# Optimization experiments

Hardware: AMD Instinct MI355X
Metric: run time of the kernel (lower is better)

Reference implementation:

```python
import jax, jax.numpy as jnp
import numpy as np

B, N, K = 2, 8192, 9
FEAT_C, COST_C, FLOW_C = 128, 64, 3
CH = [128, 128]          # PointConv output channels
MLP = [128, 64]          # pointwise Conv1d channels
WN = 16                  # WeightNet output width
HID = [8, 8]             # WeightNet hidden widths
SLOPE = 0.1              # leaky relu slope
EPS = 1e-5
CLAMP = (-200.0, 200.0)


def setup_inputs() -> dict:
    key = jax.random.key(0)
    ks = iter(jax.random.split(key, 64))
    def nrm(shape, s=0.02):
        return jax.random.normal(next(ks), shape, jnp.float32) * s
    inp = {}
    inp["xyz"] = jax.random.normal(next(ks), (B, N, 3), jnp.float32)
    inp["feats"] = jax.random.normal(next(ks), (B, FEAT_C, N), jnp.float32)
    inp["cost_volume"] = jax.random.normal(next(ks), (B, COST_C, N), jnp.float32)
    inp["flow"] = jax.random.normal(next(ks), (B, FLOW_C, N), jnp.float32)
    last = FEAT_C + COST_C + FLOW_C
    for i, co in enumerate(CH):
        cin = last + 3
        p = f"pc{i}_"
        inp[p + "w1"] = nrm((HID[0], 3)); inp[p + "b1"] = jnp.zeros((HID[0],), jnp.float32)
        inp[p + "w2"] = nrm((HID[1], HID[0])); inp[p + "b2"] = jnp.zeros((HID[1],), jnp.float32)
        inp[p + "w3"] = nrm((WN, HID[1])); inp[p + "b3"] = jnp.zeros((WN,), jnp.float32)
        inp[p + "linW"] = nrm((co, cin * WN)); inp[p + "linb"] = jnp.zeros((co,), jnp.float32)
        last = co
    for i, co in enumerate(MLP):
        inp[f"mlp{i}_W"] = nrm((co, last)); inp[f"mlp{i}_b"] = jnp.zeros((co,), jnp.float32)
        last = co
    inp["fc_W"] = nrm((3, last)); inp["fc_b"] = jnp.zeros((3,), jnp.float32)
    return inp


def _bn(x, axes):
    m = x.mean(axes, keepdims=True)
    v = x.var(axes, keepdims=True)
    return (x - m) / jnp.sqrt(v + EPS)


def _leaky(x):
    return jnp.where(x >= 0, x, SLOPE * x)


def _knn_idx(xyz, k):
    # xyz: [B,N,3] -> idx [B,N,K] of k nearest (incl. self)
    sq = jnp.sum(xyz * xyz, -1)                       # [B,N]
    d = sq[:, :, None] + sq[:, None, :] - 2.0 * jnp.einsum('bnc,bmc->bnm', xyz, xyz)
    return jax.lax.top_k(-d, k)[1]                    # [B,N,K]


def _gather(a, idx):
    # a: [B,N,C], idx: [B,N,K] -> [B,N,K,C]
    return jax.vmap(lambda x, i: x[i])(a, idx)


def _pointconv(xyz, points, idx, w1, b1, w2, b2, w3, b3, linW, linb):
    # xyz [B,N,3], points [B,C,N] -> [B,out,N]
    g_xyz = _gather(xyz, idx) - xyz[:, :, None, :]    # [B,N,K,3] relative coords
    g_pts = _gather(jnp.transpose(points, (0, 2, 1)), idx)  # [B,N,K,C]
    grouped = jnp.concatenate([g_pts, g_xyz], -1)     # [B,N,K,C+3]
    # WeightNet on relative coords: 3 -> 8 -> 8 -> 16 (bn+relu each)
    h = jax.nn.relu(_bn(g_xyz @ w1.T + b1, (0, 1, 2)))
    h = jax.nn.relu(_bn(h @ w2.T + b2, (0, 1, 2)))
    w = jax.nn.relu(_bn(h @ w3.T + b3, (0, 1, 2)))    # [B,N,K,WN]
    bsz, n = grouped.shape[0], grouped.shape[1]
    agg = jnp.einsum('bnkc,bnkw->bncw', grouped, w).reshape(bsz, n, -1)
    out = agg @ linW.T + linb                         # [B,N,out]
    out = _leaky(_bn(out, (0, 1)))
    return jnp.transpose(out, (0, 2, 1))              # [B,out,N]


def reference(xyz, feats, cost_volume, flow,
              pc0_w1, pc0_b1, pc0_w2, pc0_b2, pc0_w3, pc0_b3, pc0_linW, pc0_linb,
              pc1_w1, pc1_b1, pc1_w2, pc1_b2, pc1_w3, pc1_b3, pc1_linW, pc1_linb,
              mlp0_W, mlp0_b, mlp1_W, mlp1_b, fc_W, fc_b):
    idx = _knn_idx(xyz, K)
    x = jnp.concatenate([feats, cost_volume, flow], axis=1)  # [B, feat+cost+flow, N]
    x = _pointconv(xyz, x, idx, pc0_w1, pc0_b1, pc0_w2, pc0_b2, pc0_w3, pc0_b3, pc0_linW, pc0_linb)
    x = _pointconv(xyz, x, idx, pc1_w1, pc1_b1, pc1_w2, pc1_b2, pc1_w3, pc1_b3, pc1_linW, pc1_linb)
    x = _leaky(jnp.einsum('oc,bcn->bon', mlp0_W, x) + mlp0_b[None, :, None])
    x = _leaky(jnp.einsum('oc,bcn->bon', mlp1_W, x) + mlp1_b[None, :, None])
    fl = jnp.einsum('oc,bcn->bon', fc_W, x) + fc_b[None, :, None]
    return x, jnp.clip(fl, CLAMP[0], CLAMP[1])
```

## Files before the change

kernel.cpp:

```cpp
#include <hip/hip_runtime.h>

#define NBATCH 2
#define NPTS   8192
#define NPT    (NBATCH*NPTS)
#define KNN    9
#define SEG    32
#define SEGN   (NPTS/SEG)
#define SCAP   8
#define SSTR   9

typedef unsigned short u16;
typedef unsigned int   u32;
typedef short bf16x8 __attribute__((ext_vector_type(8)));
typedef float f32x4  __attribute__((ext_vector_type(4)));

__device__ __forceinline__ float wred(float v){
#pragma unroll
  for(int o=32;o>0;o>>=1) v += __shfl_down(v,o);
  return v;
}

__device__ __forceinline__ u16 f2b(float f){
  u32 u = __float_as_uint(f);
  return (u16)((u + 0x7fffu + ((u>>16)&1u)) >> 16);
}

__device__ __forceinline__ float bumpup(float x){
  u32 u = __float_as_uint(x);
  if(u == 0x80000000u) u = 1u;
  else if((int)u >= 0) u += 1u;
  else u -= 1u;
  return __uint_as_float(u);
}

__global__ __launch_bounds__(256) void k_build_xin(
    const float* __restrict__ feats, const float* __restrict__ cost,
    const float* __restrict__ flow, const float* __restrict__ xyz,
    float* __restrict__ xin, float4* __restrict__ xs)
{
  __shared__ float buf[196][67];
  int t = threadIdx.x;
  int pt0 = blockIdx.x*64;
  int b = pt0 >> 13, n0 = pt0 & (NPTS-1);
  int lane = t & 63, grp = t >> 6;
  const float* f  = feats + (size_t)b*128*NPTS + n0 + lane;
  const float* cv = cost  + (size_t)b*64 *NPTS + n0 + lane;
  const float* fl = flow  + (size_t)b*3  *NPTS + n0 + lane;
  for(int c=grp; c<128; c+=4) buf[c][lane]      = f[(size_t)c*NPTS];
  for(int c=grp; c<64;  c+=4) buf[128+c][lane]  = cv[(size_t)c*NPTS];
  if(grp<3) buf[192+grp][lane] = fl[(size_t)grp*NPTS];
  else      buf[195][lane] = 0.f;
  if(t < 64){
    int pt = pt0 + t;
    const float* p = xyz + (size_t)b*NPTS*3 + 3*(pt & (NPTS-1));
    float x=p[0], y=p[1], z=p[2];
    float s = __fadd_rn(__fadd_rn(__fmul_rn(x,x),__fmul_rn(y,y)),__fmul_rn(z,z));
    xs[pt] = make_float4(x,y,z,s);
  }
  __syncthreads();
  for(int e=t; e<64*49; e+=256){
    int p = e/49, q = e-p*49;
    float4 v = make_float4(buf[4*q][p], buf[4*q+1][p], buf[4*q+2][p], buf[4*q+3][p]);
    *(float4*)(xin + (size_t)(pt0+p)*196 + 4*q) = v;
  }
}

__global__ __launch_bounds__(256) void k_thr(
    const float4* __restrict__ xs, float* __restrict__ thr)
{
  __shared__ float md[4][64][9];
  int t = threadIdx.x, lane = t & 63, wave = t >> 6;
  int qb = blockIdx.x;
  int b = qb >> 7;
  int n = (qb & 127)*64 + lane;
  const float4* xb4 = xs + (size_t)b*NPTS;
  float4 q = xb4[n];
  float qx=q.x, qy=q.y, qz=q.z, qs=q.w;
  float bd[KNN];
#pragma unroll
  for(int i=0;i<KNN;i++) bd[i]=__builtin_inff();
  for(int i=0;i<128;i++){
    int m = (wave*128 + i)*16;
    float4 c = xb4[m];
    float dot = fmaf(c.z,qz, fmaf(c.y,qy, __fmul_rn(c.x,qx)));
    float d = __fsub_rn(__fadd_rn(qs,c.w), __fmul_rn(2.0f,dot));
    if(d < bd[KNN-1]){
      bd[KNN-1]=d;
#pragma unroll
      for(int r=KNN-2;r>=0;r--){
        if(bd[r+1] < bd[r]){ float td=bd[r]; bd[r]=bd[r+1]; bd[r+1]=td; }
      }
    }
  }
#pragma unroll
  for(int i=0;i<KNN;i++) md[wave][lane][i]=bd[i];
  __syncthreads();
  if(t < 64){
    float b2[KNN];
#pragma unroll
    for(int i=0;i<KNN;i++) b2[i]=__builtin_inff();
    for(int w=0;w<4;w++){
#pragma unroll
      for(int i=0;i<KNN;i++){
        float d = md[w][t][i];
        if(d < b2[KNN-1]){
          b2[KNN-1]=d;
#pragma unroll
          for(int r=KNN-2;r>=0;r--){
            if(b2[r+1] < b2[r]){ float td=b2[r]; b2[r]=b2[r+1]; b2[r+1]=td; }
          }
        }
      }
    }
    thr[(b<<13) + (qb & 127)*64 + t] = b2[KNN-1];
  }
}

__global__ __launch_bounds__(256) void k_knn_part(
    const float4* __restrict__ xs, const float* __restrict__ thr,
    int* __restrict__ pi)
{
  __shared__ int sqi[256*SSTR];
  int t = threadIdx.x;
  int seg = blockIdx.x & (SEG-1);
  int qc  = blockIdx.x >> 5;
  int b = qc >> 5;
  int n = (qc & 31)*256 + t;
  int pt = (b<<13) + n;
  const float4* xb4 = xs + (size_t)b*NPTS;
  float4 q = xb4[n];
  float qx=q.x, qy=q.y, qz=q.z, qs=q.w;
  float init = bumpup(thr[pt]);
  float bd[KNN]; int bi[KNN];
#pragma unroll
  for(int i=0;i<KNN;i++){ bd[i]=init; bi[i]=0x7fffffff; }
  float cut = init;
  int cnt = 0;
  int* msi = sqi + t*SSTR;
  auto flush = [&](){
    for(int i=0;i<cnt;i++){
      int id = msi[i];
      float4 c = xb4[id];
      float dot = fmaf(c.z,qz, fmaf(c.y,qy, __fmul_rn(c.x,qx)));
      float d = __fsub_rn(__fadd_rn(qs,c.w), __fmul_rn(2.0f,dot));
      if(d < bd[KNN-1]){
        bd[KNN-1]=d; bi[KNN-1]=id;
#pragma unroll
        for(int r=KNN-2;r>=0;r--){
          if(bd[r+1] < bd[r]){
            float td=bd[r]; bd[r]=bd[r+1]; bd[r+1]=td;
            int ti=bi[r]; bi[r]=bi[r+1]; bi[r+1]=ti;
          }
        }
      }
    }
    cnt = 0;
    cut = bd[KNN-1];
  };
  const int m0 = seg*SEGN;
  for(int j0=0; j0<SEGN; j0+=8){
    float dv[8];
#pragma unroll
    for(int u=0;u<8;u++){
      float4 c = xb4[m0+j0+u];
      float dot = fmaf(c.z,qz, fmaf(c.y,qy, __fmul_rn(c.x,qx)));
      dv[u] = __fsub_rn(__fadd_rn(qs,c.w), __fmul_rn(2.0f,dot));
    }
#pragma unroll
    for(int u=0;u<8;u++){
      if(dv[u] < cut){
        msi[cnt] = m0+j0+u; cnt++;
        if(cnt==SCAP) flush();
      }
    }
  }
  flush();
  size_t base = ((size_t)pt*SEG + seg)*KNN;
#pragma unroll
  for(int i=0;i<KNN;i++) pi[base+i]=bi[i];
}

__global__ __launch_bounds__(256) void k_knn_merge(
    const float4* __restrict__ xs, const int* __restrict__ pi,
    int* __restrict__ idxo, float* __restrict__ gpart)
{
  __shared__ float red[4][9];
  int t = threadIdx.x;
  int pt = blockIdx.x*256 + t;
  int b = pt >> 13;
  const float4* xb4 = xs + (size_t)b*NPTS;
  float4 q = xb4[pt & (NPTS-1)];
  float qx=q.x, qy=q.y, qz=q.z, qs=q.w;
  const int4* ip = (const int4*)(pi + (size_t)pt*SEG*KNN);
  float bd[KNN]; int bi[KNN];
#pragma unroll
  for(int i=0;i<KNN;i++){ bd[i]=__builtin_inff(); bi[i]=0x7fffffff; }
  for(int v=0; v<SEG*KNN/4; v++){
    int4 iv = ip[v];
    int ii[4] = {iv.x,iv.y,iv.z,iv.w};
#pragma unroll
    for(int u=0;u<4;u++){
      int id = ii[u];
      if(id != 0x7fffffff){
        float4 c = xb4[id];
        float dot = fmaf(c.z,qz, fmaf(c.y,qy, __fmul_rn(c.x,qx)));
        float d = __fsub_rn(__fadd_rn(qs,c.w), __fmul_rn(2.0f,dot));
        if(d < bd[KNN-1]){
          bd[KNN-1]=d; bi[KNN-1]=id;
#pragma unroll
          for(int i=KNN-2;i>=0;i--){
            if(bd[i+1] < bd[i]){
              float td=bd[i]; bd[i]=bd[i+1]; bd[i+1]=td;
              int ti=bi[i]; bi[i]=bi[i+1]; bi[i+1]=ti;
            }
          }
        }
      }
    }
  }
#pragma unroll
  for(int r=0;r<KNN;r++) idxo[pt*KNN + r] = bi[r];
  float mom[9];
#pragma unroll
  for(int i=0;i<9;i++) mom[i]=0.f;
#pragma unroll
  for(int r=0;r<KNN;r++){
    int m = bi[r];
    float4 c = xb4[m];
    float gx=c.x-qx, gy=c.y-qy, gz=c.z-qz;
    mom[0]+=gx; mom[1]+=gy; mom[2]+=gz;
    mom[3]=fmaf(gx,gx,mom[3]); mom[4]=fmaf(gy,gy,mom[4]); mom[5]=fmaf(gz,gz,mom[5]);
    mom[6]=fmaf(gx,gy,mom[6]); mom[7]=fmaf(gx,gz,mom[7]); mom[8]=fmaf(gy,gz,mom[8]);
  }
  int wave = t>>6, lane = t&63;
#pragma unroll
  for(int i=0;i<9;i++){
    float s = wred(mom[i]);
    if(lane==0) red[wave][i]=s;
  }
  __syncthreads();
  if(t<9)
    gpart[blockIdx.x*9 + t] = red[0][t]+red[1][t]+red[2][t]+red[3][t];
}

__global__ __launch_bounds__(256) void k_wn23a2(
    const float* __restrict__ xyz, const int* __restrict__ idx,
    const float* __restrict__ gpart, float cnt,
    const float* __restrict__ W1a, const float* __restrict__ B1a,
    const float* __restrict__ W2a, const float* __restrict__ B2a,
    const float* __restrict__ W1b, const float* __restrict__ B1b,
    const float* __restrict__ W2b, const float* __restrict__ B2b,
    float* __restrict__ houta, float* __restrict__ houtb,
    float* __restrict__ parta, float* __restrict__ partb)
{
  __shared__ float mom[9];
  __shared__ float stl[2][16];
  __shared__ float red[4][2][8];
  int t = threadIdx.x;
  if(t<9){
    float s=0.f;
    for(int r=0;r<64;r++) s += gpart[r*9+t];
    mom[t]=s;
  }
  __syncthreads();
  if(t<16){
    int L = t>>3, j = t&7;
    const float* W1 = L? W1b : W1a;
    const float* B1 = L? B1b : B1a;
    float inv = 1.0f/cnt;
    float w0=W1[3*j], w1=W1[3*j+1], w2=W1[3*j+2], bb=B1[j];
    float Eg0=mom[0]*inv, Eg1=mom[1]*inv, Eg2=mom[2]*inv;
    float Mxx=mom[3]*inv, Myy=mom[4]*inv, Mzz=mom[5]*inv;
    float Mxy=mom[6]*inv, Mxz=mom[7]*inv, Myz=mom[8]*inv;
    float mu_lin = w0*Eg0 + w1*Eg1 + w2*Eg2;
    float mean = mu_lin + bb;
    float e2 = w0*w0*Mxx + w1*w1*Myy + w2*w2*Mzz
             + 2.f*(w0*w1*Mxy + w0*w2*Mxz + w1*w2*Myz)
             + 2.f*bb*mu_lin + bb*bb;
    float var = e2 - mean*mean;
    stl[L][j] = mean;
    stl[L][8+j] = 1.0f/sqrtf(var + 1e-5f);
  }
  __syncthreads();
  int e = blockIdx.x*256 + t;
  int pt = e/KNN;
  int b = pt>>13, n = pt & (NPTS-1);
  int m = idx[e];
  const float* xb = xyz + (size_t)b*NPTS*3;
  float gx = xb[3*m]-xb[3*n], gy = xb[3*m+1]-xb[3*n+1], gz = xb[3*m+2]-xb[3*n+2];
  int wave = t>>6, lane = t&63;
#pragma unroll
  for(int L=0; L<2; L++){
    const float* W1 = L? W1b : W1a;
    const float* B1 = L? B1b : B1a;
    const float* W2 = L? W2b : W2a;
    const float* B2 = L? B2b : B2a;
    float* hout = L? houtb : houta;
    float* part = L? partb : parta;
    float x[8];
#pragma unroll
    for(int j=0;j<8;j++){
      float d = fmaf(gz, W1[3*j+2], fmaf(gy, W1[3*j+1], gx*W1[3*j]));
      float v = d + B1[j];
      v = (v - stl[L][j])*stl[L][8+j];
      x[j] = v>0.f? v : 0.f;
    }
    float v[8];
#pragma unroll
    for(int j=0;j<8;j++){
      float d = 0.f;
#pragma unroll
      for(int i=0;i<8;i++) d = fmaf(x[i], W2[j*8+i], d);
      v[j] = d + B2[j];
      hout[(size_t)e*8 + j] = v[j];
    }
#pragma unroll
    for(int j=0;j<8;j++){
      float s = wred(v[j]);
      float q = wred(v[j]*v[j]);
      if(lane==0){ red[wave][0][j]=s; red[wave][1][j]=q; }
    }
    __syncthreads();
    if(t < 16){
      int isq = t>>3, c = t&7;
      part[blockIdx.x*16 + t] =
        red[0][isq][c]+red[1][isq][c]+red[2][isq][c]+red[3][isq][c];
    }
    __syncthreads();
  }
}

__global__ __launch_bounds__(256) void k_wn23_2(
    const float* __restrict__ hina, const float* __restrict__ pina,
    const float* __restrict__ hinb, const float* __restrict__ pinb,
    int nb, float cnt,
    const float* __restrict__ Wa, const float* __restrict__ Ba,
    const float* __restrict__ Wb, const float* __restrict__ Bb,
    float* __restrict__ houta, float* __restrict__ houtb,
    float* __restrict__ parta, float* __restrict__ partb)
{
  __shared__ float sa[256], qa[256];
  __shared__ float stl[16];
  __shared__ float red[4][2][16];
  int t = threadIdx.x;
  int e = blockIdx.x*256 + t;
  int wave = t>>6, lane = t&63;
#pragma unroll
  for(int L=0; L<2; L++){
    const float* hin = L? hinb : hina;
    const float* pin = L? pinb : pina;
    const float* W   = L? Wb : Wa;
    const float* Bv  = L? Bb : Ba;
    float* hout = L? houtb : houta;
    float* part = L? partb : parta;
    {
      int c = t % 8;
      int r0 = t / 8;
      float s=0.f, q=0.f;
      for(int r=r0; r<nb; r+=32){
        s += pin[r*16 + c];
        q += pin[r*16 + 8 + c];
      }
      sa[t]=s; qa[t]=q;
      __syncthreads();
      if(t < 8){
        for(int g=1; g<32; g++){ s += sa[t+g*8]; q += qa[t+g*8]; }
        float mean = s/cnt;
        float var  = q/cnt - mean*mean;
        stl[t]   = mean;
        stl[8+t] = 1.0f/sqrtf(var + 1e-5f);
      }
      __syncthreads();
    }
    float x[8];
#pragma unroll
    for(int i=0;i<8;i++){
      float v = (hin[(size_t)e*8 + i] - stl[i])*stl[8+i];
      x[i] = v>0.f? v : 0.f;
    }
    float v[16];
#pragma unroll
    for(int j=0;j<16;j++){
      float d = 0.f;
#pragma unroll
      for(int i=0;i<8;i++) d = fmaf(x[i], W[j*8+i], d);
      v[j] = d + Bv[j];
      hout[(size_t)e*16 + j] = v[j];
    }
#pragma unroll
    for(int j=0;j<16;j++){
      float s = wred(v[j]);
      float q = wred(v[j]*v[j]);
      if(lane==0){ red[wave][0][j]=s; red[wave][1][j]=q; }
    }
    __syncthreads();
    if(t < 32){
      int isq = t>>4, c = t&15;
      part[blockIdx.x*32 + t] =
        red[0][isq][c]+red[1][isq][c]+red[2][isq][c]+red[3][isq][c];
    }
    __syncthreads();
  }
}

__global__ __launch_bounds__(256) void k_fin2(
    const float* __restrict__ pa, const float* __restrict__ pb,
    float* __restrict__ sta, float* __restrict__ stb, int nb, float cnt)
{
  __shared__ float sa[256], qa[256];
  int t = threadIdx.x;
  const int C = 16;
#pragma unroll
  for(int L=0; L<2; L++){
    const float* partial = L? pb : pa;
    float* st = L? stb : sta;
    int c = t % C;
    int r0 = t / C;
    int stride = 256 / C;
    float s=0.f, q=0.f;
    for(int r=r0; r<nb; r+=stride){
      s += partial[r*2*C + c];
      q += partial[r*2*C + C + c];
    }
    sa[t]=s; qa[t]=q;
    __syncthreads();
    if(t < C){
      for(int g=1; g<stride; g++){ s += sa[t+g*C]; q += qa[t+g*C]; }
      float mean = s/cnt;
      float var  = q/cnt - mean*mean;
      st[t]   = mean;
      st[C+t] = 1.0f/sqrtf(var + 1e-5f);
    }
    __syncthreads();
  }
}

__global__ __launch_bounds__(256) void k_fin(
    const float* __restrict__ partial, float* __restrict__ st,
    int C, int nb, float cnt)
{
  __shared__ float sa[256], qa[256];
  int t = threadIdx.x;
  int c = t % C;
  int r0 = t / C;
  int stride = 256 / C;
  float s=0.f, q=0.f;
  for(int r=r0; r<nb; r+=stride){
    s += partial[r*2*C + c];
    q += partial[r*2*C + C + c];
  }
  sa[t]=s; qa[t]=q;
  __syncthreads();
  if(t < C){
    for(int g=1; g<stride; g++){ s += sa[t+g*C]; q += qa[t+g*C]; }
    float mean = s/cnt;
    float var  = q/cnt - mean*mean;
    st[t]   = mean;
    st[C+t] = 1.0f/sqrtf(var + 1e-5f);
  }
}

__global__ __launch_bounds__(256) void k_prepW2(
    const float* __restrict__ W0, u16* __restrict__ Wh0,
    const float* __restrict__ W1, u16* __restrict__ Wh1)
{
  int e = blockIdx.x*256 + threadIdx.x;
  const int N0 = 128*3200;
  if(e < N0){
    int o = e / 3200, k = e - o*3200;
    float w = (k < 3168) ? W0[o*3168 + k] : 0.f;
    Wh0[e] = f2b(w);
  } else {
    int e1 = e - N0;
    if(e1 >= 128*2112) return;
    int o = e1 / 2112, k = e1 - o*2112;
    float w = (k < 2096) ? W1[o*2096 + k] : 0.f;
    Wh1[e1] = f2b(w);
  }
}

template<int CIN, int XSTRIDE, int KP, bool BN>
__global__ __launch_bounds__(256) void k_buildA(
    const float* __restrict__ xin, const float* __restrict__ xyz,
    const int* __restrict__ idx, const float* __restrict__ wpre,
    const float* __restrict__ st3, const float* __restrict__ bnst,
    u16* __restrict__ Abuf, int c0)
{
  constexpr int P = 16;
  constexpr int CPTS = CIN-3;
  constexpr int CPAD = KP/16;
  __shared__ float wm[P][KNN][16];
  __shared__ float gxs[P][KNN][3];
  __shared__ int   si[P][KNN];
  __shared__ float sm3[16], sr3[16];
  int t = threadIdx.x;
  int pt0 = c0 + blockIdx.x*P;
  int b = pt0 >> 13;
  const float* xb = xyz + (size_t)b*NPTS*3;
  if(t<16){ sm3[t]=st3[t]; sr3[t]=st3[16+t]; }
  for(int e=t; e<P*KNN; e+=256){
    int p = e/KNN, k = e - p*KNN;
    int n = (pt0+p)&(NPTS-1);
    int m = idx[(pt0+p)*KNN+k];
    si[p][k]=m;
    gxs[p][k][0]=xb[3*m]  -xb[3*n];
    gxs[p][k][1]=xb[3*m+1]-xb[3*n+1];
    gxs[p][k][2]=xb[3*m+2]-xb[3*n+2];
  }
  __syncthreads();
  for(int e=t; e<P*KNN*16; e+=256){
    int p = e/(KNN*16); int r = e - p*(KNN*16); int k = r>>4, wn = r&15;
    float v = (wpre[((size_t)(pt0+p)*KNN + k)*16 + wn] - sm3[wn]) * sr3[wn];
    wm[p][k][wn] = v>0.f? v:0.f;
  }
  __syncthreads();
  for(int it=t; it<P*CPAD; it+=256){
    int p = it/CPAD, c = it - p*CPAD;
    u32 u[8];
    if(c < CIN){
      float g[KNN];
      if(c < CPTS){
#pragma unroll
        for(int k=0;k<KNN;k++)
          g[k] = xin[(size_t)((b<<13) + si[p][k])*XSTRIDE + c];
        if(BN){
          float sm = bnst[c], sr = bnst[128+c];
#pragma unroll
          for(int k=0;k<KNN;k++){
            float v = (g[k]-sm)*sr;
            g[k] = v>=0.f? v : 0.1f*v;
          }
        }
      } else {
        int cc = c - CPTS;
#pragma unroll
        for(int k=0;k<KNN;k++) g[k] = gxs[p][k][cc];
      }
      float a[16];
#pragma unroll
      for(int wn=0; wn<16; wn++){
        float s = 0.f;
#pragma unroll
        for(int k=0;k<KNN;k++) s = fmaf(g[k], wm[p][k][wn], s);
        a[wn] = s;
      }
#pragma unroll
      for(int j=0;j<8;j++)
        u[j] = (u32)f2b(a[2*j]) | ((u32)f2b(a[2*j+1])<<16);
    } else {
#pragma unroll
      for(int j=0;j<8;j++) u[j]=0;
    }
    u32* dst = (u32*)(Abuf + ((size_t)(blockIdx.x*P + p)*KP + c*16));
    *(uint4*)dst       = make_uint4(u[0],u[1],u[2],u[3]);
    *((uint4*)dst + 1) = make_uint4(u[4],u[5],u[6],u[7]);
  }
}

__device__ __forceinline__ void gload16(const void* g, void* l){
  __builtin_amdgcn_global_load_lds(
      (const __attribute__((address_space(1))) u32*)g,
      (__attribute__((address_space(3))) u32*)l, 16, 0, 0);
}

template<int KP>
__global__ __launch_bounds__(512) void k_gemm(
    const u16* __restrict__ Wh, const u16* __restrict__ A,
    const float* __restrict__ linb, float* __restrict__ outp,
    float* __restrict__ partial, int ptBase)
{
  __shared__ __attribute__((aligned(16))) u16 lds[24576];
  constexpr int NT = KP/64;
  int t = threadIdx.x, wave = t>>6, lane = t&63;
  int p0 = blockIdx.x*64;
  const u16* Ab = A + (size_t)p0*KP;

  auto stage = [&](const u16* __restrict__ g, int k0, int ldsByteOff, int rows){
    int nr = (rows*128) >> 13;
    for(int r=0;r<nr;r++){
      int y  = (r*8 + wave) << 10;
      int yl = y + lane*16;
      int row = yl >> 7;
      int s = (yl >> 4) & 7;
      int c = s ^ (row & 7);
      const u16* src = g + (size_t)row*KP + k0 + c*8;
      gload16(src, (char*)lds + ldsByteOff + y);
    }
  };

  stage(Wh, 0, 0,     128);
  stage(Ab, 0, 32768, 64);

  f32x4 acc[4];
#pragma unroll
  for(int j=0;j<4;j++) acc[j]=(f32x4)(0.f);

  for(int kt=0; kt<NT; kt++){
    int cur = kt & 1;
    __syncthreads();
    if(kt+1 < NT){
      int nxt = cur^1;
      stage(Wh, (kt+1)*64, nxt*16384,         128);
      stage(Ab, (kt+1)*64, 32768 + nxt*8192,  64);
    }
    const u16* Lw = lds + cur*8192;
    const u16* La = lds + 16384 + cur*4096;
#pragma unroll
    for(int kf=0; kf<2; kf++){
      int cb = kf*4 + (lane>>4);
      bf16x8 af[4];
#pragma unroll
      for(int nf=0; nf<4; nf++){
        int p = nf*16 + (lane&15);
        af[nf] = *(const bf16x8*)(La + p*64 + ((cb ^ (p&7))<<3));
      }
      int row = wave*16 + (lane&15);
      bf16x8 wh = *(const bf16x8*)(Lw + row*64 + ((cb ^ (row&7))<<3));
#pragma unroll
      for(int nf=0; nf<4; nf++)
        acc[nf] = __builtin_amdgcn_mfma_f32_16x16x32_bf16(wh, af[nf], acc[nf], 0,0,0);
    }
  }

  int gb = (ptBase>>6) + blockIdx.x;
  int q = lane>>4, lc = lane&15;
  int obase = wave*16 + q*4;
#pragma unroll
  for(int r=0;r<4;r++){
    int o = obase + r;
    float bo = linb[o];
    float sv = 0.f, qv = 0.f;
#pragma unroll
    for(int nf=0; nf<4; nf++){
      float x = acc[nf][r] + bo;
      outp[(size_t)(ptBase + p0 + nf*16 + lc)*128 + o] = x;
      sv += x; qv = fmaf(x,x,qv);
    }
#pragma unroll
    for(int off=8; off>0; off>>=1){
      sv += __shfl_down(sv,off);
      qv += __shfl_down(qv,off);
    }
    if(lc==0){
      partial[gb*256 + o]       = sv;
      partial[gb*256 + 128 + o] = qv;
    }
  }
}

__global__ __launch_bounds__(512) void k_mlp(
    const float* __restrict__ outp1, const float* __restrict__ sto,
    const float* __restrict__ W0, const float* __restrict__ B0,
    const float* __restrict__ W1, const float* __restrict__ B1,
    const float* __restrict__ Wf, const float* __restrict__ Bf,
    float* __restrict__ dout)
{
  __shared__ float w0l[128*129];
  __shared__ float w1l[128*65];
  __shared__ float xt [128*65];
  __shared__ float m1l[64*65];
  int t = threadIdx.x;
  int pt0 = blockIdx.x*64;
  int b = pt0 >> 13, n0 = pt0 & (NPTS-1);
  for(int e=t; e<128*128; e+=512){ int o=e>>7, j=e&127; w0l[j*129+o] = W0[e]; }
  for(int e=t; e<64*128;  e+=512){ int o=e>>7, j=e&127; w1l[j*65+o]  = W1[e]; }
  for(int e=t; e<64*128;  e+=512){
    int p=e>>7, j=e&127;
    float v = outp1[(size_t)(pt0+p)*128 + j];
    v = (v - sto[j])*sto[128+j];
    xt[j*65+p] = v>=0.f? v : 0.1f*v;
  }
  __syncthreads();
  int p = t&63, wv = t>>6;
  float acc[16];
#pragma unroll
  for(int i=0;i<16;i++) acc[i]=0.f;
  for(int j=0;j<128;j++){
    float xv = xt[j*65+p];
#pragma unroll
    for(int i=0;i<16;i++)
      acc[i] = fmaf(w0l[j*129 + wv*16 + i], xv, acc[i]);
  }
  __syncthreads();
#pragma unroll
  for(int i=0;i<16;i++){
    int o = wv*16+i;
    float v = acc[i] + B0[o];
    v = v>=0.f? v : 0.1f*v;
    xt[o*65 + p] = v;
  }
  __syncthreads();
  float a2[8];
#pragma unroll
  for(int i=0;i<8;i++) a2[i]=0.f;
  for(int j=0;j<128;j++){
    float xv = xt[j*65+p];
#pragma unroll
    for(int i=0;i<8;i++)
      a2[i] = fmaf(w1l[j*65 + wv*8 + i], xv, a2[i]);
  }
#pragma unroll
  for(int i=0;i<8;i++){
    int o = wv*8+i;
    float v = a2[i] + B1[o];
    v = v>=0.f? v : 0.1f*v;
    dout[(size_t)(b*64+o)*NPTS + n0 + p] = v;
    m1l[o*65+p] = v;
  }
  __syncthreads();
  if(t < 192){
    int o = t/64, pp = t%64;
    float a = Bf[o];
    for(int j=0;j<64;j++) a = fmaf(Wf[o*64+j], m1l[j*65+pp], a);
    a = fminf(fmaxf(a, -200.f), 200.f);
    dout[(size_t)NBATCH*64*NPTS + (size_t)(b*3+o)*NPTS + n0 + pp] = a;
  }
}

extern "C" void kernel_launch(void* const* d_in, const int* in_sizes, int n_in,
                              void* d_out, int out_size, void* d_ws, size_t ws_size,
                              hipStream_t stream)
{
  (void)in_sizes; (void)n_in; (void)out_size;
  const float* xyz   = (const float*)d_in[0];
  const float* feats = (const float*)d_in[1];
  const float* cost  = (const float*)d_in[2];
  const float* flow  = (const float*)d_in[3];
  const float* pw1[2]  = {(const float*)d_in[4],  (const float*)d_in[12]};
  const float* pb1[2]  = {(const float*)d_in[5],  (const float*)d_in[13]};
  const float* pw2[2]  = {(const float*)d_in[6],  (const float*)d_in[14]};
  const float* pb2[2]  = {(const float*)d_in[7],  (const float*)d_in[15]};
  const float* pw3[2]  = {(const float*)d_in[8],  (const float*)d_in[16]};
  const float* pb3[2]  = {(const float*)d_in[9],  (const float*)d_in[17]};
  const float* plW[2]  = {(const float*)d_in[10], (const float*)d_in[18]};
  const float* plb[2]  = {(const float*)d_in[11], (const float*)d_in[19]};
  const float* m0W = (const float*)d_in[20];
  const float* m0b = (const float*)d_in[21];
  const float* m1W = (const float*)d_in[22];
  const float* m1b = (const float*)d_in[23];
  const float* fcW = (const float*)d_in[24];
  const float* fcb = (const float*)d_in[25];
  float* out = (float*)d_out;

  const int KP0 = 3200;
  const int KP1 = 2112;

  float* ws = (float*)d_ws;
  size_t o = 0;
  float* xin0 = ws + o; o += (size_t)NPT*196;
  int*   idx  = (int*)(ws + o); o += (size_t)NPT*KNN + 3;
  o &= ~(size_t)3;
  float4* xs  = (float4*)(ws + o); o += (size_t)NPT*4;
  float* thr  = ws + o; o += (size_t)NPT;
  int*   pi   = (int*)(ws + o); o += (size_t)NPT*SEG*KNN;
  float* h2a  = ws + o; o += (size_t)NPT*KNN*8;
  float* h2b  = ws + o; o += (size_t)NPT*KNN*8;
  float* wpre0 = ws + o; o += (size_t)NPT*KNN*16;
  float* wpre1 = ws + o; o += (size_t)NPT*KNN*16;
  float* gpart = ws + o; o += 64*9 + 7;
  float* part2a = ws + o; o += 576*16;
  float* part2b = ws + o; o += 576*16;
  float* part3a = ws + o; o += 576*32;
  float* part3b = ws + o; o += 576*32;
  float* parto = ws + o; o += 65536;
  float* st3a = ws + o; o += 32;
  float* st3b = ws + o; o += 32;
  float* sto0 = ws + o; o += 256;
  float* sto1 = ws + o; o += 256;
  float* outp0 = ws + o; o += (size_t)NPT*128;
  float* outp1 = ws + o; o += (size_t)NPT*128;
  u16* Wh0 = (u16*)(ws + o); o += (size_t)128*KP0/2;
  u16* Wh1 = (u16*)(ws + o); o += (size_t)128*KP1/2;
  u16* Abuf = (u16*)(ws + o);
  size_t used_bytes = o*4;
  size_t avail = ws_size > used_bytes ? ws_size - used_bytes : 0;
  int npc = NPT;
  while(npc > 1024 && (size_t)npc*KP0*2 > avail) npc >>= 1;

  k_build_xin<<<NPT/64, 256, 0, stream>>>(feats, cost, flow, xyz, xin0, xs);
  k_thr<<<256, 256, 0, stream>>>(xs, thr);
  k_knn_part<<<64*SEG, 256, 0, stream>>>(xs, thr, pi);
  k_knn_merge<<<NPT/256, 256, 0, stream>>>(xs, pi, idx, gpart);

  k_prepW2<<<(128*(KP0+KP1)+255)/256, 256, 0, stream>>>(plW[0], Wh0, plW[1], Wh1);

  const float cnt1 = (float)(NPT*KNN);
  const float cnto = (float)NPT;

  k_wn23a2<<<576,256,0,stream>>>(xyz, idx, gpart, cnt1,
                                 pw1[0], pb1[0], pw2[0], pb2[0],
                                 pw1[1], pb1[1], pw2[1], pb2[1],
                                 h2a, h2b, part2a, part2b);
  k_wn23_2<<<576,256,0,stream>>>(h2a, part2a, h2b, part2b, 576, cnt1,
                                 pw3[0], pb3[0], pw3[1], pb3[1],
                                 wpre0, wpre1, part3a, part3b);
  k_fin2<<<1,256,0,stream>>>(part3a, part3b, st3a, st3b, 576, cnt1);

  for(int c0 = 0; c0 < NPT; c0 += npc){
    k_buildA<198,196,KP0,false><<<npc/16,256,0,stream>>>(xin0, xyz, idx, wpre0, st3a, sto0, Abuf, c0);
    k_gemm<KP0><<<npc/64,512,0,stream>>>(Wh0, Abuf, plb[0], outp0, parto, c0);
  }
  k_fin<<<1,256,0,stream>>>(parto, sto0, 128, NPT/64, cnto);

  for(int c0 = 0; c0 < NPT; c0 += npc){
    k_buildA<131,128,KP1,true><<<npc/16,256,0,stream>>>(outp0, xyz, idx, wpre1, st3b, sto0, Abuf, c0);
    k_gemm<KP1><<<npc/64,512,0,stream>>>(Wh1, Abuf, plb[1], outp1, parto, c0);
  }
  k_fin<<<1,256,0,stream>>>(parto, sto1, 128, NPT/64, cnto);

  k_mlp<<<NPT/64,512,0,stream>>>(outp1, sto1, m0W,m0b, m1W,m1b, fcW,fcb, out);
}
```

Measured before the change: 580.1 us.

## Restructure KNN stages: finer threshold split, fewer segments, cache candidate distances

The threshold kernel now gives each query 16 threads instead of 4, so it launches more blocks and fills the GPU better. The partial KNN pass drops from 32 to 16 segments and keeps candidate distances in shared memory, so flushes no longer reload coordinates or recompute distances. It also writes partial distances along with indices, which lets the merge kernel skip its own gathers and distance math. In exchange there is an extra distance buffer in global memory, more shared memory per block, and each segment scans longer.

```diff
diff --git a/kernel.cpp b/kernel.cpp
--- a/kernel.cpp
+++ b/kernel.cpp
@@ -4,10 +4,9 @@
 #define NPTS   8192
 #define NPT    (NBATCH*NPTS)
 #define KNN    9
-#define SEG    32
+#define SEG    16
 #define SEGN   (NPTS/SEG)
-#define SCAP   8
-#define SSTR   9
+#define SSTR   20
 
 typedef unsigned short u16;
 typedef unsigned int   u32;
@@ -68,19 +67,20 @@
 __global__ __launch_bounds__(256) void k_thr(
     const float4* __restrict__ xs, float* __restrict__ thr)
 {
-  __shared__ float md[4][64][9];
-  int t = threadIdx.x, lane = t & 63, wave = t >> 6;
+  __shared__ float md[16][16][9];
+  int t = threadIdx.x;
+  int q = t & 15, chunk = t >> 4;
   int qb = blockIdx.x;
-  int b = qb >> 7;
-  int n = (qb & 127)*64 + lane;
+  int b = qb >> 9;
+  int n = (qb & 511)*16 + q;
   const float4* xb4 = xs + (size_t)b*NPTS;
-  float4 q = xb4[n];
-  float qx=q.x, qy=q.y, qz=q.z, qs=q.w;
+  float4 Q = xb4[n];
+  float qx=Q.x, qy=Q.y, qz=Q.z, qs=Q.w;
   float bd[KNN];
 #pragma unroll
   for(int i=0;i<KNN;i++) bd[i]=__builtin_inff();
-  for(int i=0;i<128;i++){
-    int m = (wave*128 + i)*16;
+  for(int i=0;i<32;i++){
+    int m = (chunk*32 + i)*16;
     float4 c = xb4[m];
     float dot = fmaf(c.z,qz, fmaf(c.y,qy, __fmul_rn(c.x,qx)));
     float d = __fsub_rn(__fadd_rn(qs,c.w), __fmul_rn(2.0f,dot));
@@ -93,16 +93,16 @@
     }
   }
 #pragma unroll
-  for(int i=0;i<KNN;i++) md[wave][lane][i]=bd[i];
-  __syncthreads();
-  if(t < 64){
+  for(int i=0;i<KNN;i++) md[q][chunk][i]=bd[i];
+  __syncthreads();
+  if(t < 16){
     float b2[KNN];
 #pragma unroll
     for(int i=0;i<KNN;i++) b2[i]=__builtin_inff();
-    for(int w=0;w<4;w++){
+    for(int w=0;w<16;w++){
 #pragma unroll
       for(int i=0;i<KNN;i++){
-        float d = md[w][t][i];
+        float d = md[t][w][i];
         if(d < b2[KNN-1]){
           b2[KNN-1]=d;
 #pragma unroll
@@ -112,18 +112,19 @@
         }
       }
     }
-    thr[(b<<13) + (qb & 127)*64 + t] = b2[KNN-1];
+    thr[(b<<13) + (qb & 511)*16 + t] = b2[KNN-1];
   }
 }
 
 __global__ __launch_bounds__(256) void k_knn_part(
     const float4* __restrict__ xs, const float* __restrict__ thr,
-    int* __restrict__ pi)
-{
-  __shared__ int sqi[256*SSTR];
+    float* __restrict__ pd, int* __restrict__ pi)
+{
+  __shared__ float sdq[256*SSTR];
+  __shared__ int   sqi[256*SSTR];
   int t = threadIdx.x;
   int seg = blockIdx.x & (SEG-1);
-  int qc  = blockIdx.x >> 5;
+  int qc  = blockIdx.x >> 4;
   int b = qc >> 5;
   int n = (qc & 31)*256 + t;
   int pt = (b<<13) + n;
@@ -136,13 +137,11 @@
   for(int i=0;i<KNN;i++){ bd[i]=init; bi[i]=0x7fffffff; }
   float cut = init;
   int cnt = 0;
-  int* msi = sqi + t*SSTR;
+  float* msd = sdq + t*SSTR;
+  int*   msi = sqi + t*SSTR;
   auto flush = [&](){
     for(int i=0;i<cnt;i++){
-      int id = msi[i];
-      float4 c = xb4[id];
-      float dot = fmaf(c.z,qz, fmaf(c.y,qy, __fmul_rn(c.x,qx)));
-      float d = __fsub_rn(__fadd_rn(qs,c.w), __fmul_rn(2.0f,dot));
+      float d = msd[i]; int id = msi[i];
       if(d < bd[KNN-1]){
         bd[KNN-1]=d; bi[KNN-1]=id;
 #pragma unroll
@@ -159,6 +158,7 @@
   };
   const int m0 = seg*SEGN;
   for(int j0=0; j0<SEGN; j0+=8){
+    if(cnt > SSTR-8) flush();
     float dv[8];
 #pragma unroll
     for(int u=0;u<8;u++){
@@ -169,19 +169,19 @@
 #pragma unroll
     for(int u=0;u<8;u++){
       if(dv[u] < cut){
-        msi[cnt] = m0+j0+u; cnt++;
-        if(cnt==SCAP) flush();
+        msd[cnt]=dv[u]; msi[cnt]=m0+j0+u; cnt++;
       }
     }
   }
   flush();
   size_t base = ((size_t)pt*SEG + seg)*KNN;
 #pragma unroll
-  for(int i=0;i<KNN;i++) pi[base+i]=bi[i];
+  for(int i=0;i<KNN;i++){ pd[base+i]=bd[i]; pi[base+i]=bi[i]; }
 }
 
 __global__ __launch_bounds__(256) void k_knn_merge(
-    const float4* __restrict__ xs, const int* __restrict__ pi,
+    const float4* __restrict__ xs,
+    const float* __restrict__ pd, const int* __restrict__ pi,
     int* __restrict__ idxo, float* __restrict__ gpart)
 {
   __shared__ float red[4][9];
@@ -190,29 +190,26 @@
   int b = pt >> 13;
   const float4* xb4 = xs + (size_t)b*NPTS;
   float4 q = xb4[pt & (NPTS-1)];
-  float qx=q.x, qy=q.y, qz=q.z, qs=q.w;
-  const int4* ip = (const int4*)(pi + (size_t)pt*SEG*KNN);
+  const float4* dp = (const float4*)(pd + (size_t)pt*SEG*KNN);
+  const int4*   ip = (const int4*)(pi + (size_t)pt*SEG*KNN);
   float bd[KNN]; int bi[KNN];
 #pragma unroll
   for(int i=0;i<KNN;i++){ bd[i]=__builtin_inff(); bi[i]=0x7fffffff; }
   for(int v=0; v<SEG*KNN/4; v++){
-    int4 iv = ip[v];
-    int ii[4] = {iv.x,iv.y,iv.z,iv.w};
+    float4 dv = dp[v];
+    int4   iv = ip[v];
+    float dd[4] = {dv.x,dv.y,dv.z,dv.w};
+    int   ii[4] = {iv.x,iv.y,iv.z,iv.w};
 #pragma unroll
     for(int u=0;u<4;u++){
-      int id = ii[u];
-      if(id != 0x7fffffff){
-        float4 c = xb4[id];
-        float dot = fmaf(c.z,qz, fmaf(c.y,qy, __fmul_rn(c.x,qx)));
-        float d = __fsub_rn(__fadd_rn(qs,c.w), __fmul_rn(2.0f,dot));
-        if(d < bd[KNN-1]){
-          bd[KNN-1]=d; bi[KNN-1]=id;
-#pragma unroll
-          for(int i=KNN-2;i>=0;i--){
-            if(bd[i+1] < bd[i]){
-              float td=bd[i]; bd[i]=bd[i+1]; bd[i+1]=td;
-              int ti=bi[i]; bi[i]=bi[i+1]; bi[i+1]=ti;
-            }
+      float d = dd[u]; int id = ii[u];
+      if(d < bd[KNN-1]){
+        bd[KNN-1]=d; bi[KNN-1]=id;
+#pragma unroll
+        for(int i=KNN-2;i>=0;i--){
+          if(bd[i+1] < bd[i]){
+            float td=bd[i]; bd[i]=bd[i+1]; bd[i+1]=td;
+            int ti=bi[i]; bi[i]=bi[i+1]; bi[i+1]=ti;
           }
         }
       }
@@ -227,7 +224,7 @@
   for(int r=0;r<KNN;r++){
     int m = bi[r];
     float4 c = xb4[m];
-    float gx=c.x-qx, gy=c.y-qy, gz=c.z-qz;
+    float gx=c.x-q.x, gy=c.y-q.y, gz=c.z-q.z;
     mom[0]+=gx; mom[1]+=gy; mom[2]+=gz;
     mom[3]=fmaf(gx,gx,mom[3]); mom[4]=fmaf(gy,gy,mom[4]); mom[5]=fmaf(gz,gz,mom[5]);
     mom[6]=fmaf(gx,gy,mom[6]); mom[7]=fmaf(gx,gz,mom[7]); mom[8]=fmaf(gy,gz,mom[8]);
@@ -752,6 +749,7 @@
   o &= ~(size_t)3;
   float4* xs  = (float4*)(ws + o); o += (size_t)NPT*4;
   float* thr  = ws + o; o += (size_t)NPT;
+  float* pd   = ws + o; o += (size_t)NPT*SEG*KNN;
   int*   pi   = (int*)(ws + o); o += (size_t)NPT*SEG*KNN;
   float* h2a  = ws + o; o += (size_t)NPT*KNN*8;
   float* h2b  = ws + o; o += (size_t)NPT*KNN*8;
@@ -778,9 +776,9 @@
   while(npc > 1024 && (size_t)npc*KP0*2 > avail) npc >>= 1;
 
   k_build_xin<<<NPT/64, 256, 0, stream>>>(feats, cost, flow, xyz, xin0, xs);
-  k_thr<<<256, 256, 0, stream>>>(xs, thr);
-  k_knn_part<<<64*SEG, 256, 0, stream>>>(xs, thr, pi);
-  k_knn_merge<<<NPT/256, 256, 0, stream>>>(xs, pi, idx, gpart);
+  k_thr<<<1024, 256, 0, stream>>>(xs, thr);
+  k_knn_part<<<64*SEG, 256, 0, stream>>>(xs, thr, pd, pi);
+  k_knn_merge<<<NPT/256, 256, 0, stream>>>(xs, pd, pi, idx, gpart);
 
   k_prepW2<<<(128*(KP0+KP1)+255)/256, 256, 0, stream>>>(plW[0], Wh0, plW[1], Wh1);
 
```

Result: faster. 520.2 us (-10.3%).
